# Optimization experiments

Hardware: AMD Instinct MI355X
Metric: run time of the kernel (lower is better)

Reference implementation:

```python
import jax, jax.numpy as jnp
import numpy as np
import math

B, C, T, F_IN, F_OUT, H = 4, 8, 512, 512, 512, 8
DK = F_IN // H
NEG_SLOPE = 0.01


def _clinear(xr, xi, Wr, br, Wi, bi):
    # ComplexLinear: (fc_r(xr) - fc_i(xi), fc_r(xi) + fc_i(xr)), each fc has its own bias
    rr = xr @ Wr.T + br
    ii = xi @ Wi.T + bi
    ri = xi @ Wr.T + br
    ir = xr @ Wi.T + bi
    return rr - ii, ri + ir


def _lrelu(x):
    return jnp.where(x >= 0, x, NEG_SLOPE * x)


def setup_inputs() -> dict:
    key = jax.random.key(0)
    ks = jax.random.split(key, 32)
    d = {}
    names = ["query_r", "query_i", "key_r", "key_i", "value_r", "value_i"]
    for n, k in zip(names, ks[:6]):
        d[n] = jax.random.normal(k, (B, C, T, F_IN), dtype=jnp.float32)
    s_in = 1.0 / math.sqrt(F_IN)
    idx = 6
    for p in ["q", "k", "v"]:
        for part in ["r", "i"]:
            d[f"W{p}_{part}"] = jax.random.uniform(ks[idx], (F_IN, F_IN), jnp.float32, -s_in, s_in); idx += 1
            d[f"b{p}_{part}"] = jax.random.uniform(ks[idx], (F_IN,), jnp.float32, -s_in, s_in); idx += 1
    for part in ["r", "i"]:
        d[f"Wo_{part}"] = jax.random.uniform(ks[idx], (F_OUT, F_IN), jnp.float32, -s_in, s_in); idx += 1
        d[f"bo_{part}"] = jax.random.uniform(ks[idx], (F_OUT,), jnp.float32, -s_in, s_in); idx += 1
    return d


def reference(query_r, query_i, key_r, key_i, value_r, value_i,
              Wq_r, bq_r, Wq_i, bq_i, Wk_r, bk_r, Wk_i, bk_i,
              Wv_r, bv_r, Wv_i, bv_i, Wo_r, bo_r, Wo_i, bo_i):
    def split_heads(x):  # (B,C,T,F) -> (B,H,T,C,DK)
        return x.reshape(B, C, T, H, DK).transpose(0, 3, 2, 1, 4)

    qr, qi = _clinear(query_r, query_i, Wq_r, bq_r, Wq_i, bq_i)
    kr, ki = _clinear(key_r, key_i, Wk_r, bk_r, Wk_i, bk_i)
    vr, vi = _clinear(value_r, value_i, Wv_r, bv_r, Wv_i, bv_i)
    qr, qi, kr, ki, vr, vi = map(split_heads, (qr, qi, kr, ki, vr, vi))
    vr, vi = _lrelu(vr), _lrelu(vi)

    # conjugate_transpose_matmul_conjugate: scores over channel dim (B,H,T,C,C)
    qk = lambda a, b: jnp.einsum('bhtcd,bhted->bhtce', a, b)
    scale = 1.0 / math.sqrt(DK)
    sr = (qk(qr, kr) + qk(qi, ki)) * scale
    si = (-qk(qi, kr) + qk(qr, ki)) * scale

    # complex matmul scores @ v (dropout p=0 is identity)
    av = lambda s, v: jnp.einsum('bhtce,bhted->bhtcd', s, v)
    xr = av(sr, vr) - av(si, vi)
    xi = av(si, vr) + av(sr, vi)

    def merge_heads(x):  # (B,H,T,C,DK) -> (B,C,T,H*DK)
        return x.transpose(0, 3, 2, 1, 4).reshape(B, C, T, H * DK)

    xr, xi = _lrelu(merge_heads(xr)), _lrelu(merge_heads(xi))
    return _clinear(xr, xi, Wo_r, bo_r, Wo_i, bo_i)
```

## Files before the change

### kernel.cpp

```cpp
#include <hip/hip_runtime.h>

#define B_  4
#define C_  8
#define T_  512
#define F_  512
#define H_  8
#define M_  (B_*C_*T_)

typedef unsigned short u16;
typedef unsigned int   u32;
typedef __bf16 bf16x8 __attribute__((ext_vector_type(8)));
typedef float  f32x4  __attribute__((ext_vector_type(4)));

__device__ __forceinline__ float bf2f(u16 s) {
    union { u32 u; float f; } c; c.u = ((u32)s) << 16; return c.f;
}
__device__ __forceinline__ u16 f2bf(float f) {
    union { float f; u32 u; } c; c.f = f;
    u32 r = c.u + 0x7fffu + ((c.u >> 16) & 1u);
    return (u16)(r >> 16);
}
__device__ __forceinline__ float bflo(u32 v){ union{u32 u; float f;} c; c.u = v << 16;        return c.f; }
__device__ __forceinline__ float bfhi(u32 v){ union{u32 u; float f;} c; c.u = v & 0xffff0000u; return c.f; }

__device__ __forceinline__ void async16(u16* lds, const u16* g) {
    __builtin_amdgcn_global_load_lds(
        (const __attribute__((address_space(1))) u32*)g,
        (__attribute__((address_space(3))) u32*)lds,
        16, 0, 0);
}

struct ConvArgs { const float* src[6]; u16* dst[6]; };

__global__ __launch_bounds__(256)
void convert6_kernel(ConvArgs a)
{
    const int tid  = threadIdx.x;
    const int base = blockIdx.x * 1024 + tid;
    const float4* s = (const float4*)a.src[blockIdx.y];
    uint4*        d = (uint4*)a.dst[blockIdx.y];

    float4 v[8];
    #pragma unroll
    for (int k = 0; k < 4; ++k) {
        const int o = base + (k << 8);
        v[2*k]     = s[2*o];
        v[2*k + 1] = s[2*o + 1];
    }
    #pragma unroll
    for (int k = 0; k < 4; ++k) {
        const int o = base + (k << 8);
        uint4 u;
        u.x = (u32)f2bf(v[2*k].x)   | ((u32)f2bf(v[2*k].y)   << 16);
        u.y = (u32)f2bf(v[2*k].z)   | ((u32)f2bf(v[2*k].w)   << 16);
        u.z = (u32)f2bf(v[2*k+1].x) | ((u32)f2bf(v[2*k+1].y) << 16);
        u.w = (u32)f2bf(v[2*k+1].z) | ((u32)f2bf(v[2*k+1].w) << 16);
        d[o] = u;
    }
}

struct PrepArgs { const float* wr[4]; const float* wi[4]; const float* br[4]; const float* bi[4]; };

__global__ __launch_bounds__(256)
void prep_weights_kernel(PrepArgs a, u16* __restrict__ wbig, float* __restrict__ bbig)
{
    const int s   = blockIdx.y;
    const int idx = blockIdx.x * 256 + threadIdx.x;
    const int n   = idx >> 8;
    const int k0  = (idx & 255) << 2;
    const int nn = n & 511, kk = k0 & 511;
    const float* src; float sgn = 1.0f;
    if (n < 512) { if (k0 < 512) src = a.wr[s]; else { src = a.wi[s]; sgn = -1.0f; } }
    else         { if (k0 < 512) src = a.wi[s]; else   src = a.wr[s]; }
    const float4 v = *(const float4*)(src + (size_t)nn * 512 + kk);
    ushort4 q;
    q.x = f2bf(sgn * v.x); q.y = f2bf(sgn * v.y);
    q.z = f2bf(sgn * v.z); q.w = f2bf(sgn * v.w);
    *(ushort4*)(wbig + (size_t)s * 1048576 + (size_t)n * 1024 + k0) = q;

    if (blockIdx.x < 4) {
        const int bidx = blockIdx.x * 256 + threadIdx.x;
        const float brv = a.br[s][bidx & 511];
        const float biv = a.bi[s][bidx & 511];
        bbig[s * 1024 + bidx] = (bidx < 512) ? (brv - biv) : (brv + biv);
    }
}

template <bool PERM_OUT, bool LRELU, bool OUT_F32>
__global__ __launch_bounds__(256, 4)
void mfma_clinear_kernel(const u16* __restrict__ Ar, const u16* __restrict__ Ai,
                         const u16* __restrict__ Wbt, const float* __restrict__ bias,
                         void* __restrict__ Yr_, void* __restrict__ Yi_)
{
    constexpr int SMEM_ELEMS = PERM_OUT ? (128 * 136) : (128 * 128);
    __shared__ __align__(16) u16 smem[SMEM_ELEMS];
    u16* sA = smem;
    u16* sB = smem + 8192;

    const int tid  = threadIdx.x;
    const int wave = tid >> 6;
    const int lane = tid & 63;
    const int m0   = blockIdx.x << 7;
    const int n0   = blockIdx.y << 7;
    const int mw   = (wave >> 1) << 6;
    const int nw   = (wave & 1) << 6;

    const int srow = tid >> 2;
    const int sk   = (tid & 3) << 3;
    const size_t arow0 = (size_t)(m0 + srow) * 512;
    const size_t arow1 = (size_t)(m0 + 64 + srow) * 512;
    const size_t brow0 = (size_t)(n0 + srow) * 1024;
    const size_t brow1 = (size_t)(n0 + 64 + srow) * 1024;

    u16* ldsA = sA + (wave << 9);
    u16* ldsB = sB + (wave << 9);

    f32x4 acc[4][4] = {};

    const int fr = lane & 15;
    const int fq = (lane >> 4) << 3;

    for (int k0 = 0; k0 < 1024; k0 += 64) {
        const u16* As = (k0 < 512) ? Ar : Ai;
        const int  ak = (k0 & 511) + sk;
        __syncthreads();
        #pragma unroll
        for (int p = 0; p < 2; ++p) {
            const int kp = p << 5;
            async16(ldsA + p * 4096,        As + arow0 + ak + kp);
            async16(ldsA + p * 4096 + 2048, As + arow1 + ak + kp);
            async16(ldsB + p * 4096,        Wbt + brow0 + k0 + sk + kp);
            async16(ldsB + p * 4096 + 2048, Wbt + brow1 + k0 + sk + kp);
        }
        __syncthreads();

        #pragma unroll
        for (int p = 0; p < 2; ++p) {
            bf16x8 af[4], bfr[4];
            #pragma unroll
            for (int i = 0; i < 4; ++i)
                af[i] = *(const bf16x8*)&sA[p * 4096 + (mw + i * 16 + fr) * 32 + fq];
            #pragma unroll
            for (int j = 0; j < 4; ++j)
                bfr[j] = *(const bf16x8*)&sB[p * 4096 + (nw + j * 16 + fr) * 32 + fq];

            #pragma unroll
            for (int i = 0; i < 4; ++i)
                #pragma unroll
                for (int j = 0; j < 4; ++j)
                    acc[i][j] = __builtin_amdgcn_mfma_f32_16x16x32_bf16(af[i], bfr[j], acc[i][j], 0, 0, 0);
        }
    }

    const int col_l = lane & 15;
    const int row_l = (lane >> 4) << 2;

    if constexpr (PERM_OUT) {
        constexpr int LDN = 136;
        __syncthreads();
        #pragma unroll
        for (int j = 0; j < 4; ++j) {
            const int ncl = nw + (j << 4) + col_l;
            const float bv = bias[n0 + ncl];
            #pragma unroll
            for (int i = 0; i < 4; ++i) {
                const int mrow = mw + (i << 4) + row_l;
                #pragma unroll
                for (int r = 0; r < 4; ++r) {
                    float v = acc[i][j][r] + bv;
                    if constexpr (LRELU) v = v >= 0.f ? v : 0.01f * v;
                    smem[(mrow + r) * LDN + ncl] = f2bf(v);
                }
            }
        }
        __syncthreads();
        u16* Yr = (u16*)Yr_;
        u16* Yi = (u16*)Yi_;
        #pragma unroll
        for (int s = 0; s < 8; ++s) {
            const int idx = (s << 8) + tid;
            const int ml  = idx >> 4;
            const int c8  = (idx & 15) << 3;
            const uint4 dv = *(const uint4*)&smem[ml * LDN + c8];
            const int m    = m0 + ml;
            const int ncol = n0 + c8;
            const int part = ncol >> 9;
            const int nc   = ncol & 511;
            const int bb = m >> 12, cc = (m >> 9) & 7, tt = m & 511;
            const int hh = nc >> 6, dd = nc & 63;
            const size_t addr = ((size_t)(((bb << 3) + hh) * T_ + tt) << 9) + (cc << 6) + dd;
            u16* Y = part ? Yi : Yr;
            *(uint4*)(Y + addr) = dv;
        }
    } else {
        #pragma unroll
        for (int j = 0; j < 4; ++j) {
            const int ncol = n0 + nw + (j << 4) + col_l;
            const float bv = bias[ncol];
            const int part = ncol >> 9;
            const int nc   = ncol & 511;
            float* Y = part ? (float*)Yi_ : (float*)Yr_;
            #pragma unroll
            for (int i = 0; i < 4; ++i) {
                const int mbase = m0 + mw + (i << 4) + row_l;
                #pragma unroll
                for (int r = 0; r < 4; ++r) {
                    float v = acc[i][j][r] + bv;
                    if constexpr (LRELU) v = v >= 0.f ? v : 0.01f * v;
                    Y[(size_t)(mbase + r) * 512 + nc] = v;
                }
            }
        }
    }
}

__global__ __launch_bounds__(256)
void attn_kernel(const u16* __restrict__ qr, const u16* __restrict__ qi,
                 const u16* __restrict__ kr, const u16* __restrict__ ki,
                 const u16* __restrict__ vr, const u16* __restrict__ vi,
                 u16* __restrict__ xr, u16* __restrict__ xi)
{
    constexpr int RS = 68;
    constexpr int MS = 8 * RS;
    __shared__ float L[4][6 * MS];
    __shared__ float S[4][128];

    const int wave = threadIdx.x >> 6;
    const int lane = threadIdx.x & 63;
    const int w    = (blockIdx.x << 2) + wave;
    const int cl   = lane >> 3;
    const int dl   = lane & 7;
    const int d0   = dl << 3;

    float* Lw = L[wave];
    const u16* srcs[6] = {qr, qi, kr, ki, vr, vi};
    const size_t gbase = ((size_t)w << 9) + (lane << 3);
    #pragma unroll
    for (int m2 = 0; m2 < 6; ++m2) {
        const uint4 u = *(const uint4*)(srcs[m2] + gbase);
        float* dst = Lw + m2 * MS + cl * RS + d0;
        dst[0]=bflo(u.x); dst[1]=bfhi(u.x);
        dst[2]=bflo(u.y); dst[3]=bfhi(u.y);
        dst[4]=bflo(u.z); dst[5]=bfhi(u.z);
        dst[6]=bflo(u.w); dst[7]=bfhi(u.w);
    }
    __syncthreads();

    {
        const float* Qr = Lw + 0*MS + cl*RS;
        const float* Qi = Lw + 1*MS + cl*RS;
        const float* Kr = Lw + 2*MS + dl*RS;
        const float* Ki = Lw + 3*MS + dl*RS;
        float srr=0.f, sii=0.f, sri=0.f, sir=0.f;
        #pragma unroll 8
        for (int d = 0; d < 64; ++d) {
            srr = fmaf(Qr[d], Kr[d], srr);
            sii = fmaf(Qi[d], Ki[d], sii);
            sri = fmaf(Qr[d], Ki[d], sri);
            sir = fmaf(Qi[d], Kr[d], sir);
        }
        S[wave][lane]      = (srr + sii) * 0.125f;
        S[wave][64 + lane] = (sri - sir) * 0.125f;
    }
    __syncthreads();

    const float* Vr = Lw + 4*MS;
    const float* Vi = Lw + 5*MS;
    const float* Sr = S[wave];
    const float* Si = S[wave] + 64;
    float outr[8] = {}, outi[8] = {};
    #pragma unroll
    for (int e = 0; e < 8; ++e) {
        const float sre = Sr[(cl<<3) + e];
        const float sie = Si[(cl<<3) + e];
        const float* vre = Vr + e*RS + d0;
        const float* vie = Vi + e*RS + d0;
        #pragma unroll
        for (int j = 0; j < 8; ++j) {
            outr[j] = fmaf(sre,  vre[j], outr[j]);
            outr[j] = fmaf(-sie, vie[j], outr[j]);
            outi[j] = fmaf(sie,  vre[j], outi[j]);
            outi[j] = fmaf(sre,  vie[j], outi[j]);
        }
    }

    const int tt = w & 511, hh = (w >> 9) & 7, bb = w >> 12;
    const size_t obase = ((size_t)(((bb << 3) + cl) * T_ + tt) << 9) + (hh << 6) + d0;
    u32 pr[4], pi[4];
    #pragma unroll
    for (int jj = 0; jj < 4; ++jj) {
        float r0 = outr[2*jj], r1 = outr[2*jj+1];
        float i0 = outi[2*jj], i1 = outi[2*jj+1];
        r0 = r0 >= 0.f ? r0 : 0.01f*r0;  r1 = r1 >= 0.f ? r1 : 0.01f*r1;
        i0 = i0 >= 0.f ? i0 : 0.01f*i0;  i1 = i1 >= 0.f ? i1 : 0.01f*i1;
        pr[jj] = (u32)f2bf(r0) | ((u32)f2bf(r1) << 16);
        pi[jj] = (u32)f2bf(i0) | ((u32)f2bf(i1) << 16);
    }
    *(uint4*)(xr + obase) = make_uint4(pr[0], pr[1], pr[2], pr[3]);
    *(uint4*)(xi + obase) = make_uint4(pi[0], pi[1], pi[2], pi[3]);
}

extern "C" void kernel_launch(void* const* d_in, const int* in_sizes, int n_in,
                              void* d_out, int out_size, void* d_ws, size_t ws_size,
                              hipStream_t stream)
{
    (void)in_sizes; (void)n_in; (void)out_size; (void)ws_size;
    const float* act[6];
    for (int i = 0; i < 6; ++i) act[i] = (const float*)d_in[i];

    PrepArgs pa;
    for (int s = 0; s < 4; ++s) {
        pa.wr[s] = (const float*)d_in[6 + s*4 + 0];
        pa.br[s] = (const float*)d_in[6 + s*4 + 1];
        pa.wi[s] = (const float*)d_in[6 + s*4 + 2];
        pa.bi[s] = (const float*)d_in[6 + s*4 + 3];
    }

    const size_t SZ = (size_t)M_ * F_;
    u16* ws = (u16*)d_ws;
    u16* a0 = ws + 0*SZ;  u16* a1 = ws + 1*SZ;
    u16* a2 = ws + 2*SZ;  u16* a3 = ws + 3*SZ;
    u16* a4 = ws + 4*SZ;  u16* a5 = ws + 5*SZ;
    u16* q0 = ws + 6*SZ;  u16* q1 = ws + 7*SZ;
    u16*   wbig = ws + 8*SZ;
    float* bbig = (float*)(wbig + 4u*1024*1024);

    ConvArgs ca;
    ca.src[0]=act[0]; ca.src[1]=act[1]; ca.src[2]=act[2];
    ca.src[3]=act[3]; ca.src[4]=act[4]; ca.src[5]=act[5];
    ca.dst[0]=a0; ca.dst[1]=a1; ca.dst[2]=a2; ca.dst[3]=a3; ca.dst[4]=a4; ca.dst[5]=a5;

    convert6_kernel<<<dim3(1024, 6), 256, 0, stream>>>(ca);
    prep_weights_kernel<<<dim3(1024, 4), 256, 0, stream>>>(pa, wbig, bbig);

    dim3 ggrid(M_/128, 1024/128);
    mfma_clinear_kernel<true,  false, false><<<ggrid, 256, 0, stream>>>(
        a0, a1, wbig + 0u*1048576, bbig + 0*1024, q0, q1);
    mfma_clinear_kernel<true,  false, false><<<ggrid, 256, 0, stream>>>(
        a2, a3, wbig + 1u*1048576, bbig + 1*1024, a0, a1);
    mfma_clinear_kernel<true,  true,  false><<<ggrid, 256, 0, stream>>>(
        a4, a5, wbig + 2u*1048576, bbig + 2*1024, a2, a3);

    attn_kernel<<<dim3((B_*H_*T_)/4), 256, 0, stream>>>(q0, q1, a0, a1, a2, a3, a4, a5);

    float* out_r = (float*)d_out;
    mfma_clinear_kernel<false, false, true><<<ggrid, 256, 0, stream>>>(
        a4, a5, wbig + 3u*1048576, bbig + 3*1024, out_r, out_r + SZ);
}
```

Measured before the change: 470.2 us.

## Rewrite complex-linear GEMM with 256x256 tiles, double-buffered LDS and XOR swizzle

```diff
diff --git a/kernel.cpp b/kernel.cpp
--- a/kernel.cpp
+++ b/kernel.cpp
@@ -86,128 +86,168 @@
     }
 }
 
-template <bool PERM_OUT, bool LRELU, bool OUT_F32>
-__global__ __launch_bounds__(256, 4)
-void mfma_clinear_kernel(const u16* __restrict__ Ar, const u16* __restrict__ Ai,
-                         const u16* __restrict__ Wbt, const float* __restrict__ bias,
-                         void* __restrict__ Yr_, void* __restrict__ Yi_)
-{
-    constexpr int SMEM_ELEMS = PERM_OUT ? (128 * 136) : (128 * 128);
-    __shared__ __align__(16) u16 smem[SMEM_ELEMS];
-    u16* sA = smem;
-    u16* sB = smem + 8192;
+template <bool PERM_OUT, bool LRELU>
+__global__ __launch_bounds__(512, 2)
+void mfma_clinear256_kernel(const u16* __restrict__ Ar, const u16* __restrict__ Ai,
+                            const u16* __restrict__ Wbt, const float* __restrict__ bias,
+                            void* __restrict__ Yr_, void* __restrict__ Yi_)
+{
+    constexpr int SMEM_U16 = PERM_OUT ? (256 * 272) : (256 * 256);
+    __shared__ __align__(16) u16 smem[SMEM_U16];
+    char* const sm = (char*)smem;
 
     const int tid  = threadIdx.x;
-    const int wave = tid >> 6;
+    const int wv   = tid >> 6;
     const int lane = tid & 63;
-    const int m0   = blockIdx.x << 7;
-    const int n0   = blockIdx.y << 7;
-    const int mw   = (wave >> 1) << 6;
-    const int nw   = (wave & 1) << 6;
-
-    const int srow = tid >> 2;
-    const int sk   = (tid & 3) << 3;
-    const size_t arow0 = (size_t)(m0 + srow) * 512;
-    const size_t arow1 = (size_t)(m0 + 64 + srow) * 512;
-    const size_t brow0 = (size_t)(n0 + srow) * 1024;
-    const size_t brow1 = (size_t)(n0 + 64 + srow) * 1024;
-
-    u16* ldsA = sA + (wave << 9);
-    u16* ldsB = sB + (wave << 9);
-
-    f32x4 acc[4][4] = {};
-
-    const int fr = lane & 15;
-    const int fq = (lane >> 4) << 3;
-
-    for (int k0 = 0; k0 < 1024; k0 += 64) {
-        const u16* As = (k0 < 512) ? Ar : Ai;
-        const int  ak = (k0 & 511) + sk;
+    const int m0   = blockIdx.x << 8;
+    const int n0   = blockIdx.y << 8;
+    const int wm   = (wv >> 2) << 7;
+    const int wn   = (wv & 3) << 6;
+
+    const int frow = lane & 15;
+    const int fkb  = (lane >> 4) << 4;
+
+    const int srow = tid >> 3;
+    const int scol = ((tid & 7) ^ (srow & 7)) << 3;
+    const int ldst = wv << 10;
+
+    f32x4 acc[8][4] = {};
+    bf16x8 bq[4][2];
+
+    {
+        #pragma unroll
+        for (int b = 0; b < 4; ++b)
+            async16((u16*)(sm + 65536 + b * 8192 + ldst),
+                    Wbt + (size_t)(n0 + b * 64 + srow) * 1024 + scol);
+        async16((u16*)(sm + 0 * 8192 + ldst), Ar + (size_t)(m0 +   0 + srow) * 512 + scol);
+        async16((u16*)(sm + 2 * 8192 + ldst), Ar + (size_t)(m0 + 128 + srow) * 512 + scol);
+        async16((u16*)(sm + 1 * 8192 + ldst), Ar + (size_t)(m0 +  64 + srow) * 512 + scol);
+        async16((u16*)(sm + 3 * 8192 + ldst), Ar + (size_t)(m0 + 192 + srow) * 512 + scol);
+        asm volatile("s_waitcnt vmcnt(2)" ::: "memory");
+        asm volatile("s_barrier" ::: "memory");
+    }
+
+    for (int tt = 0; tt < 16; ++tt) {
+        char* const curA = sm + ((tt & 1) << 15);
+        char* const curB = sm + 65536 + ((tt & 1) << 15);
+        char* const nxtA = sm + (((tt + 1) & 1) << 15);
+        char* const nxtB = sm + 65536 + (((tt + 1) & 1) << 15);
+        const bool more = (tt + 1) < 16;
+        const u16* An  = ((tt + 1) < 8) ? Ar : Ai;
+        const int  akc = ((tt + 1) & 7) << 6;
+        const int  bkc = (tt + 1) << 6;
+
+        #pragma unroll
+        for (int q = 0; q < 4; ++q) {
+            bf16x8 aq[2][2];
+            #pragma unroll
+            for (int i = 0; i < 2; ++i) {
+                const int ra = wm + (2 * q + i) * 16 + frow;
+                #pragma unroll
+                for (int kk = 0; kk < 2; ++kk) {
+                    const int cb = (kk << 6) + fkb;
+                    aq[i][kk] = *(const bf16x8*)(curA + ra * 128 + (cb ^ ((ra & 7) << 4)));
+                }
+            }
+            if (q == 0) {
+                #pragma unroll
+                for (int nf = 0; nf < 4; ++nf) {
+                    const int rb = wn + nf * 16 + frow;
+                    #pragma unroll
+                    for (int kk = 0; kk < 2; ++kk) {
+                        const int cb = (kk << 6) + fkb;
+                        bq[nf][kk] = *(const bf16x8*)(curB + rb * 128 + (cb ^ ((rb & 7) << 4)));
+                    }
+                }
+            }
+            if (more) {
+                if (q == 0) {
+                    async16((u16*)(nxtB + 0 * 8192 + ldst), Wbt + (size_t)(n0 +   0 + srow) * 1024 + bkc + scol);
+                    async16((u16*)(nxtB + 1 * 8192 + ldst), Wbt + (size_t)(n0 +  64 + srow) * 1024 + bkc + scol);
+                } else if (q == 1) {
+                    async16((u16*)(nxtB + 2 * 8192 + ldst), Wbt + (size_t)(n0 + 128 + srow) * 1024 + bkc + scol);
+                    async16((u16*)(nxtB + 3 * 8192 + ldst), Wbt + (size_t)(n0 + 192 + srow) * 1024 + bkc + scol);
+                } else if (q == 2) {
+                    async16((u16*)(nxtA + 0 * 8192 + ldst), An + (size_t)(m0 +   0 + srow) * 512 + akc + scol);
+                    async16((u16*)(nxtA + 2 * 8192 + ldst), An + (size_t)(m0 + 128 + srow) * 512 + akc + scol);
+                } else {
+                    async16((u16*)(nxtA + 1 * 8192 + ldst), An + (size_t)(m0 +  64 + srow) * 512 + akc + scol);
+                    async16((u16*)(nxtA + 3 * 8192 + ldst), An + (size_t)(m0 + 192 + srow) * 512 + akc + scol);
+                }
+            }
+            asm volatile("s_barrier" ::: "memory");
+            __builtin_amdgcn_s_setprio(1);
+            #pragma unroll
+            for (int kk = 0; kk < 2; ++kk)
+                #pragma unroll
+                for (int i = 0; i < 2; ++i)
+                    #pragma unroll
+                    for (int nf = 0; nf < 4; ++nf)
+                        acc[2 * q + i][nf] = __builtin_amdgcn_mfma_f32_16x16x32_bf16(
+                            aq[i][kk], bq[nf][kk], acc[2 * q + i][nf], 0, 0, 0);
+            __builtin_amdgcn_s_setprio(0);
+            if (q == 1) {
+                if (more) asm volatile("s_waitcnt vmcnt(4)" ::: "memory");
+                else      asm volatile("s_waitcnt vmcnt(0)" ::: "memory");
+            } else if (q == 3) {
+                if (more) asm volatile("s_waitcnt vmcnt(2)" ::: "memory");
+                else      asm volatile("s_waitcnt vmcnt(0)" ::: "memory");
+            }
+            asm volatile("s_barrier" ::: "memory");
+        }
+    }
+
+    const int row_l = (lane >> 4) << 2;
+
+    if constexpr (PERM_OUT) {
+        constexpr int LDN = 272;
+        #pragma unroll
+        for (int mf = 0; mf < 8; ++mf) {
+            const int mr = wm + mf * 16 + row_l;
+            #pragma unroll
+            for (int nf = 0; nf < 4; ++nf) {
+                const int ncl = wn + nf * 16 + frow;
+                const float bv = bias[n0 + ncl];
+                #pragma unroll
+                for (int r = 0; r < 4; ++r) {
+                    float v = acc[mf][nf][r] + bv;
+                    if constexpr (LRELU) v = v >= 0.f ? v : 0.01f * v;
+                    smem[(mr + r) * LDN + ncl] = f2bf(v);
+                }
+            }
+        }
         __syncthreads();
-        #pragma unroll
-        for (int p = 0; p < 2; ++p) {
-            const int kp = p << 5;
-            async16(ldsA + p * 4096,        As + arow0 + ak + kp);
-            async16(ldsA + p * 4096 + 2048, As + arow1 + ak + kp);
-            async16(ldsB + p * 4096,        Wbt + brow0 + k0 + sk + kp);
-            async16(ldsB + p * 4096 + 2048, Wbt + brow1 + k0 + sk + kp);
-        }
-        __syncthreads();
-
-        #pragma unroll
-        for (int p = 0; p < 2; ++p) {
-            bf16x8 af[4], bfr[4];
+        const int part = n0 >> 9;
+        u16* Y = part ? (u16*)Yi_ : (u16*)Yr_;
+        #pragma unroll
+        for (int it = 0; it < 16; ++it) {
+            const int idx = (it << 9) + tid;
+            const int ml  = idx >> 5;
+            const int c8  = (idx & 31) << 3;
+            const uint4 dv = *(const uint4*)&smem[ml * LDN + c8];
+            const int m  = m0 + ml;
+            const int nc = (n0 + c8) & 511;
+            const int bb = m >> 12, cc = (m >> 9) & 7, tq = m & 511;
+            const int hh = nc >> 6, dd = nc & 63;
+            const size_t addr = ((size_t)(((bb << 3) + hh) * T_ + tq) << 9) + (cc << 6) + dd;
+            *(uint4*)(Y + addr) = dv;
+        }
+    } else {
+        const int part = n0 >> 9;
+        float* Y = part ? (float*)Yi_ : (float*)Yr_;
+        #pragma unroll
+        for (int nf = 0; nf < 4; ++nf) {
+            const int ncol = n0 + wn + nf * 16 + frow;
+            const float bv = bias[ncol];
+            const int nc = ncol & 511;
             #pragma unroll
-            for (int i = 0; i < 4; ++i)
-                af[i] = *(const bf16x8*)&sA[p * 4096 + (mw + i * 16 + fr) * 32 + fq];
-            #pragma unroll
-            for (int j = 0; j < 4; ++j)
-                bfr[j] = *(const bf16x8*)&sB[p * 4096 + (nw + j * 16 + fr) * 32 + fq];
-
-            #pragma unroll
-            for (int i = 0; i < 4; ++i)
-                #pragma unroll
-                for (int j = 0; j < 4; ++j)
-                    acc[i][j] = __builtin_amdgcn_mfma_f32_16x16x32_bf16(af[i], bfr[j], acc[i][j], 0, 0, 0);
-        }
-    }
-
-    const int col_l = lane & 15;
-    const int row_l = (lane >> 4) << 2;
-
-    if constexpr (PERM_OUT) {
-        constexpr int LDN = 136;
-        __syncthreads();
-        #pragma unroll
-        for (int j = 0; j < 4; ++j) {
-            const int ncl = nw + (j << 4) + col_l;
-            const float bv = bias[n0 + ncl];
-            #pragma unroll
-            for (int i = 0; i < 4; ++i) {
-                const int mrow = mw + (i << 4) + row_l;
+            for (int mf = 0; mf < 8; ++mf) {
+                const int mb = m0 + wm + mf * 16 + row_l;
                 #pragma unroll
                 for (int r = 0; r < 4; ++r) {
-                    float v = acc[i][j][r] + bv;
+                    float v = acc[mf][nf][r] + bv;
                     if constexpr (LRELU) v = v >= 0.f ? v : 0.01f * v;
-                    smem[(mrow + r) * LDN + ncl] = f2bf(v);
-                }
-            }
-        }
-        __syncthreads();
-        u16* Yr = (u16*)Yr_;
-        u16* Yi = (u16*)Yi_;
-        #pragma unroll
-        for (int s = 0; s < 8; ++s) {
-            const int idx = (s << 8) + tid;
-            const int ml  = idx >> 4;
-            const int c8  = (idx & 15) << 3;
-            const uint4 dv = *(const uint4*)&smem[ml * LDN + c8];
-            const int m    = m0 + ml;
-            const int ncol = n0 + c8;
-            const int part = ncol >> 9;
-            const int nc   = ncol & 511;
-            const int bb = m >> 12, cc = (m >> 9) & 7, tt = m & 511;
-            const int hh = nc >> 6, dd = nc & 63;
-            const size_t addr = ((size_t)(((bb << 3) + hh) * T_ + tt) << 9) + (cc << 6) + dd;
-            u16* Y = part ? Yi : Yr;
-            *(uint4*)(Y + addr) = dv;
-        }
-    } else {
-        #pragma unroll
-        for (int j = 0; j < 4; ++j) {
-            const int ncol = n0 + nw + (j << 4) + col_l;
-            const float bv = bias[ncol];
-            const int part = ncol >> 9;
-            const int nc   = ncol & 511;
-            float* Y = part ? (float*)Yi_ : (float*)Yr_;
-            #pragma unroll
-            for (int i = 0; i < 4; ++i) {
-                const int mbase = m0 + mw + (i << 4) + row_l;
-                #pragma unroll
-                for (int r = 0; r < 4; ++r) {
-                    float v = acc[i][j][r] + bv;
-                    if constexpr (LRELU) v = v >= 0.f ? v : 0.01f * v;
-                    Y[(size_t)(mbase + r) * 512 + nc] = v;
+                    Y[(size_t)(mb + r) * 512 + nc] = v;
                 }
             }
         }
@@ -333,17 +373,17 @@
     convert6_kernel<<<dim3(1024, 6), 256, 0, stream>>>(ca);
     prep_weights_kernel<<<dim3(1024, 4), 256, 0, stream>>>(pa, wbig, bbig);
 
-    dim3 ggrid(M_/128, 1024/128);
-    mfma_clinear_kernel<true,  false, false><<<ggrid, 256, 0, stream>>>(
+    dim3 ggrid(M_/256, 1024/256);
+    mfma_clinear256_kernel<true,  false><<<ggrid, 512, 0, stream>>>(
         a0, a1, wbig + 0u*1048576, bbig + 0*1024, q0, q1);
-    mfma_clinear_kernel<true,  false, false><<<ggrid, 256, 0, stream>>>(
+    mfma_clinear256_kernel<true,  false><<<ggrid, 512, 0, stream>>>(
         a2, a3, wbig + 1u*1048576, bbig + 1*1024, a0, a1);
-    mfma_clinear_kernel<true,  true,  false><<<ggrid, 256, 0, stream>>>(
+    mfma_clinear256_kernel<true,  true ><<<ggrid, 512, 0, stream>>>(
         a4, a5, wbig + 2u*1048576, bbig + 2*1024, a2, a3);
 
     attn_kernel<<<dim3((B_*H_*T_)/4), 256, 0, stream>>>(q0, q1, a0, a1, a2, a3, a4, a5);
 
     float* out_r = (float*)d_out;
-    mfma_clinear_kernel<false, false, true><<<ggrid, 256, 0, stream>>>(
+    mfma_clinear256_kernel<false, false><<<ggrid, 512, 0, stream>>>(
         a4, a5, wbig + 3u*1048576, bbig + 3*1024, out_r, out_r + SZ);
 }
```

Result: faster. 441.9 us (-6.0%).
